# Optimization experiments

Measured on AMD Instinct MI355X. Metric: run time of the kernel, lower is better.

## Reference

```python
import jax, jax.numpy as jnp
import numpy as np

N_NODES = 50000
N_EDGES = 1600000
IN_FEAT = 256
HIDDEN = 128
N_CLASSES = 16


def gcn_conv(x, edge_index, W, b, n_nodes):
    """PyG GCNConv: x' = D^{-1/2} (A+I) D^{-1/2} (x @ W) + b."""
    h = x @ W  # project first (PyG order), messages are in out_dim
    src, dst = edge_index[0], edge_index[1]
    loops = jnp.arange(n_nodes, dtype=src.dtype)
    src = jnp.concatenate([src, loops])
    dst = jnp.concatenate([dst, loops])
    # degree of A+I (count incoming edges incl. self loop)
    deg = jax.ops.segment_sum(jnp.ones_like(dst, dtype=h.dtype), dst, num_segments=n_nodes)
    dis = jax.lax.rsqrt(deg)  # deg >= 1 thanks to self loops
    norm = dis[src] * dis[dst]  # [E+N]
    msgs = h[src] * norm[:, None]  # gather + scale
    out = jax.ops.segment_sum(msgs, dst, num_segments=n_nodes)  # scatter-add
    return out + b


def setup_inputs() -> dict:
    key = jax.random.key(0)
    k_x, k_e, k_w1, k_b1, k_w2, k_b2 = jax.random.split(key, 6)
    x = jax.random.normal(k_x, (N_NODES, IN_FEAT), dtype=jnp.float32)
    edge_index = jax.random.randint(k_e, (2, N_EDGES), 0, N_NODES, dtype=jnp.int64)
    s1 = 1.0 / np.sqrt(IN_FEAT)
    s2 = 1.0 / np.sqrt(HIDDEN)
    W1 = jax.random.uniform(k_w1, (IN_FEAT, HIDDEN), jnp.float32, -s1, s1)
    b1 = jax.random.uniform(k_b1, (HIDDEN,), jnp.float32, -s1, s1)
    W2 = jax.random.uniform(k_w2, (HIDDEN, N_CLASSES), jnp.float32, -s2, s2)
    b2 = jax.random.uniform(k_b2, (N_CLASSES,), jnp.float32, -s2, s2)
    return {"x": x, "edge_index": edge_index, "W1": W1, "b1": b1, "W2": W2, "b2": b2}


def reference(x, edge_index, W1, b1, W2, b2):
    n = x.shape[0]
    h = gcn_conv(x, edge_index, W1, b1, n)
    h = jax.nn.relu(h)
    logits = gcn_conv(h, edge_index, W2, b2, n)
    return logits, jax.nn.softmax(logits, axis=1)
```

## Files before the change

### kernel.cpp

```cpp
#include <hip/hip_runtime.h>
#include <hip/hip_bf16.h>
#include <math.h>

#define N_NODES 50000
#define N_EDGES 1600000
#define IN_FEAT 256
#define HIDDEN 128
#define N_CLASSES 16

#define ECHUNK 8192
#define NCHK 196
#define NBKT 196
#define BCAP 10240

typedef __attribute__((ext_vector_type(8))) short short8;
typedef __attribute__((ext_vector_type(4))) float floatx4;

__device__ __forceinline__ unsigned short f2bf(float f) {
    unsigned u = __float_as_uint(f);
    return (unsigned short)((u + 0x7fffu + ((u >> 16) & 1u)) >> 16);
}

__device__ __forceinline__ unsigned pk2bf(float a, float b) {
    __hip_bfloat162 h = __float22bfloat162_rn(make_float2(a, b));
    union { __hip_bfloat162 h; unsigned u; } cv;
    cv.h = h;
    return cv.u;
}

__device__ __forceinline__ float bflo(unsigned u) { return __uint_as_float(u << 16); }
__device__ __forceinline__ float bfhi(unsigned u) { return __uint_as_float(u & 0xffff0000u); }

__global__ __launch_bounds__(256) void scatter_edges2(const int* __restrict__ src,
                                                      const int* __restrict__ dst,
                                                      int* __restrict__ cursor,
                                                      unsigned int* __restrict__ sorted,
                                                      const float* __restrict__ W1,
                                                      unsigned short* __restrict__ w1t) {
    __shared__ int hloc[256];
    int t = threadIdx.x;
    hloc[t] = 0;
    if (blockIdx.x < HIDDEN)
        w1t[blockIdx.x * IN_FEAT + t] = f2bf(W1[t * HIDDEN + blockIdx.x]);
    __syncthreads();
    int base = blockIdx.x * ECHUNK;
    int end = min(base + ECHUNK, N_EDGES);
    for (int i = base + t; i < end; i += 256)
        atomicAdd(&hloc[dst[i] >> 8], 1);
    __syncthreads();
    int cnt = hloc[t];
    int lbase = t * BCAP + atomicAdd(&cursor[t], cnt);
    __syncthreads();
    hloc[t] = lbase;
    __syncthreads();
    for (int i = base + t; i < end; i += 256) {
        int d = dst[i];
        int s = src[i];
        int pos = atomicAdd(&hloc[d >> 8], 1);
        sorted[pos] = ((unsigned)d << 16) | (unsigned)s;
    }
}

__global__ __launch_bounds__(256) void build_csr2(const unsigned int* __restrict__ sorted,
                                                  const int* __restrict__ cursor,
                                                  int* __restrict__ rs,
                                                  int* __restrict__ re,
                                                  float* __restrict__ dis,
                                                  unsigned short* __restrict__ csr_src) {
    __shared__ int cnt[256];
    __shared__ int roff[256];
    int t = threadIdx.x;
    int bkt = blockIdx.x;
    int ebase = bkt * BCAP;
    int eend = ebase + cursor[bkt];
    cnt[t] = 0;
    __syncthreads();
    for (int i = ebase + t; i < eend; i += 256)
        atomicAdd(&cnt[(sorted[i] >> 16) & 255], 1);
    __syncthreads();
    int v = cnt[t];
    roff[t] = v;
    __syncthreads();
    for (int off = 1; off < 256; off <<= 1) {
        int x = (t >= off) ? roff[t - off] : 0;
        __syncthreads();
        roff[t] += x;
        __syncthreads();
    }
    int excl = roff[t] - v;
    int node = bkt * 256 + t;
    if (node < N_NODES) {
        rs[node] = ebase + excl;
        re[node] = ebase + excl + v;
        dis[node] = 1.0f / sqrtf((float)(v + 1));
    }
    __syncthreads();
    cnt[t] = ebase + excl;
    __syncthreads();
    for (int i = ebase + t; i < eend; i += 256) {
        unsigned e = sorted[i];
        int pos = atomicAdd(&cnt[(e >> 16) & 255], 1);
        csr_src[pos] = (unsigned short)(e & 0xffffu);
    }
}

#define XCH 260

__global__ __launch_bounds__(256) void gemm1_mfma(const float* __restrict__ x,
                                                  const unsigned short* __restrict__ w1t,
                                                  const float* __restrict__ dis,
                                                  unsigned int* __restrict__ g1) {
    __shared__ float xs[2][8 * XCH];
    int tid = threadIdx.x;
    int w = tid >> 6;
    int lane = tid & 63;
    int quad = lane >> 4;
    int c = lane & 15;
    int row_base = blockIdx.x * 64;
    int wrow = (w >> 1) * 32;
    int col_base = (w & 1) * 64;

    int st_row = min(row_base + 16 * w + (lane >> 3), N_NODES - 1);
    int st_row2 = min(row_base + 16 * w + 8 + (lane >> 3), N_NODES - 1);
    const float* gp1 = x + (size_t)st_row * IN_FEAT + (lane & 7) * 4;
    const float* gp2 = x + (size_t)st_row2 * IN_FEAT + (lane & 7) * 4;

    floatx4 acc[2][4] = {};
    const unsigned short* bp[4];
#pragma unroll
    for (int nt = 0; nt < 4; ++nt)
        bp[nt] = w1t + (size_t)(col_base + nt * 16 + c) * IN_FEAT + quad * 8;

    int dwoff[2];
#pragma unroll
    for (int rt = 0; rt < 2; ++rt) {
        int rit = wrow + rt * 16 + c;
        dwoff[rt] = (rit >> 3) * XCH + (rit & 7) * 32 + quad * 8;
    }

#define STAGE(buf, k0)                                                                  \
    do {                                                                                \
        __builtin_amdgcn_global_load_lds(                                               \
            (const __attribute__((address_space(1))) void*)(gp1 + (k0)),                \
            (__attribute__((address_space(3))) void*)&xs[buf][(2 * w) * XCH], 16, 0, 0);\
        __builtin_amdgcn_global_load_lds(                                               \
            (const __attribute__((address_space(1))) void*)(gp2 + (k0)),                \
            (__attribute__((address_space(3))) void*)&xs[buf][(2 * w + 1) * XCH], 16, 0, 0);\
    } while (0)

    STAGE(0, 0);
    __syncthreads();

    int buf = 0;
#pragma unroll
    for (int kk = 0; kk < 8; ++kk) {
        if (kk < 7) STAGE(buf ^ 1, (kk + 1) * 32);
        short8 b[4];
#pragma unroll
        for (int nt = 0; nt < 4; ++nt)
            b[nt] = *(const short8*)(bp[nt] + kk * 32);
        short8 a[2];
#pragma unroll
        for (int rt = 0; rt < 2; ++rt) {
            float4 f0 = *(const float4*)&xs[buf][dwoff[rt]];
            float4 f1 = *(const float4*)&xs[buf][dwoff[rt] + 4];
            union { short8 s; unsigned u[4]; } au;
            au.u[0] = pk2bf(f0.x, f0.y);
            au.u[1] = pk2bf(f0.z, f0.w);
            au.u[2] = pk2bf(f1.x, f1.y);
            au.u[3] = pk2bf(f1.z, f1.w);
            a[rt] = au.s;
        }
#pragma unroll
        for (int rt = 0; rt < 2; ++rt)
#pragma unroll
            for (int nt = 0; nt < 4; ++nt)
                acc[rt][nt] = __builtin_amdgcn_mfma_f32_16x16x32_bf16(a[rt], b[nt], acc[rt][nt], 0, 0, 0);
        __syncthreads();
        buf ^= 1;
    }
#undef STAGE

    bool evenlane = (lane & 1) == 0;
#pragma unroll
    for (int rt = 0; rt < 2; ++rt) {
#pragma unroll
        for (int reg = 0; reg < 4; ++reg) {
            int row = row_base + wrow + rt * 16 + quad * 4 + reg;
            float dv = dis[min(row, N_NODES - 1)];
#pragma unroll
            for (int nt = 0; nt < 4; ++nt) {
                float v = acc[rt][nt][reg] * dv;
                float vo = __shfl_xor(v, 1);
                if (evenlane && row < N_NODES) {
                    unsigned pkd = (unsigned)f2bf(v) | ((unsigned)f2bf(vo) << 16);
                    g1[(size_t)row * 64 + (col_base >> 1) + nt * 8 + (c >> 1)] = pkd;
                }
            }
        }
    }
}

__global__ __launch_bounds__(256) void agg1_gemm2(const unsigned int* __restrict__ g1,
                                                  const int* __restrict__ rs,
                                                  const int* __restrict__ re,
                                                  const unsigned short* __restrict__ csr_src,
                                                  const float* __restrict__ dis,
                                                  const float* __restrict__ b1,
                                                  const float* __restrict__ W2,
                                                  float* __restrict__ g2) {
    __shared__ float w2s[HIDDEN * N_CLASSES];
    __shared__ float rsh[4][HIDDEN];
    int tid = threadIdx.x;
    for (int i = tid; i < HIDDEN * N_CLASSES; i += 256) w2s[i] = W2[i];
    __syncthreads();

    int wave = tid >> 6;
    int lane = tid & 63;
    int hi = lane >> 5;
    int m = lane & 31;
    int node = blockIdx.x * 4 + wave;
    const uint2* g = (const uint2*)g1;

    float s0 = 0.f, s1 = 0.f, s2 = 0.f, s3 = 0.f;
    float t0 = 0.f, t1 = 0.f, t2 = 0.f, t3 = 0.f;
    if (hi == 0) {
        uint2 su = g[(size_t)node * 32 + m];
        s0 = bflo(su.x); s1 = bfhi(su.x); s2 = bflo(su.y); s3 = bfhi(su.y);
    }

    int e0 = rs[node], e1 = re[node];
    int e = e0;
    for (; e + 16 <= e1; e += 16) {
        int i0 = csr_src[e + 0 + hi], i1 = csr_src[e + 2 + hi];
        int i2 = csr_src[e + 4 + hi], i3 = csr_src[e + 6 + hi];
        int i4 = csr_src[e + 8 + hi], i5 = csr_src[e + 10 + hi];
        int i6 = csr_src[e + 12 + hi], i7 = csr_src[e + 14 + hi];
        uint2 u0 = g[(size_t)i0 * 32 + m];
        uint2 u1 = g[(size_t)i1 * 32 + m];
        uint2 u2 = g[(size_t)i2 * 32 + m];
        uint2 u3 = g[(size_t)i3 * 32 + m];
        uint2 u4 = g[(size_t)i4 * 32 + m];
        uint2 u5 = g[(size_t)i5 * 32 + m];
        uint2 u6 = g[(size_t)i6 * 32 + m];
        uint2 u7 = g[(size_t)i7 * 32 + m];
        s0 += bflo(u0.x); s1 += bfhi(u0.x); s2 += bflo(u0.y); s3 += bfhi(u0.y);
        t0 += bflo(u1.x); t1 += bfhi(u1.x); t2 += bflo(u1.y); t3 += bfhi(u1.y);
        s0 += bflo(u2.x); s1 += bfhi(u2.x); s2 += bflo(u2.y); s3 += bfhi(u2.y);
        t0 += bflo(u3.x); t1 += bfhi(u3.x); t2 += bflo(u3.y); t3 += bfhi(u3.y);
        s0 += bflo(u4.x); s1 += bfhi(u4.x); s2 += bflo(u4.y); s3 += bfhi(u4.y);
        t0 += bflo(u5.x); t1 += bfhi(u5.x); t2 += bflo(u5.y); t3 += bfhi(u5.y);
        s0 += bflo(u6.x); s1 += bfhi(u6.x); s2 += bflo(u6.y); s3 += bfhi(u6.y);
        t0 += bflo(u7.x); t1 += bfhi(u7.x); t2 += bflo(u7.y); t3 += bfhi(u7.y);
    }
    for (; e + 2 <= e1; e += 2) {
        int i0 = csr_src[e + hi];
        uint2 u = g[(size_t)i0 * 32 + m];
        s0 += bflo(u.x); s1 += bfhi(u.x); s2 += bflo(u.y); s3 += bfhi(u.y);
    }
    if (e < e1 && hi == 0) {
        int i0 = csr_src[e];
        uint2 u = g[(size_t)i0 * 32 + m];
        s0 += bflo(u.x); s1 += bfhi(u.x); s2 += bflo(u.y); s3 += bfhi(u.y);
    }
    s0 += t0; s1 += t1; s2 += t2; s3 += t3;
    s0 += __shfl_xor(s0, 32);
    s1 += __shfl_xor(s1, 32);
    s2 += __shfl_xor(s2, 32);
    s3 += __shfl_xor(s3, 32);

    float dv = dis[node];
    if (hi == 0) {
        float4 bb = *(const float4*)&b1[4 * m];
        float4 r;
        r.x = fmaxf(fmaf(dv, s0, bb.x), 0.f);
        r.y = fmaxf(fmaf(dv, s1, bb.y), 0.f);
        r.z = fmaxf(fmaf(dv, s2, bb.z), 0.f);
        r.w = fmaxf(fmaf(dv, s3, bb.w), 0.f);
        *(float4*)&rsh[wave][4 * m] = r;
    }

    int grp = lane >> 4;
    int c = lane & 15;
    int f0 = grp * 32;
    float p = 0.f;
#pragma unroll
    for (int k = 0; k < 32; ++k)
        p = fmaf(rsh[wave][f0 + k], w2s[(f0 + k) * N_CLASSES + c], p);
    p += __shfl_xor(p, 16);
    p += __shfl_xor(p, 32);
    if (lane < 16) g2[(size_t)node * N_CLASSES + lane] = dv * p;
}

__global__ __launch_bounds__(256) void agg2_softmax(const float* __restrict__ g2,
                                                    const int* __restrict__ rs,
                                                    const int* __restrict__ re,
                                                    const unsigned short* __restrict__ csr_src,
                                                    const float* __restrict__ dis,
                                                    const float* __restrict__ b2,
                                                    float* __restrict__ out) {
    int tid = threadIdx.x;
    int node = blockIdx.x * 16 + (tid >> 4);
    int c = tid & 15;
    float acc0 = g2[(size_t)node * N_CLASSES + c];
    float acc1 = 0.f, acc2 = 0.f, acc3 = 0.f;
    float acc4 = 0.f, acc5 = 0.f, acc6 = 0.f, acc7 = 0.f;
    int e0 = rs[node], e1 = re[node];
    int e = e0;
    for (; e + 8 <= e1; e += 8) {
        int s0 = csr_src[e + 0], s1 = csr_src[e + 1], s2 = csr_src[e + 2], s3 = csr_src[e + 3];
        int s4 = csr_src[e + 4], s5 = csr_src[e + 5], s6 = csr_src[e + 6], s7 = csr_src[e + 7];
        acc0 += g2[(size_t)s0 * N_CLASSES + c];
        acc1 += g2[(size_t)s1 * N_CLASSES + c];
        acc2 += g2[(size_t)s2 * N_CLASSES + c];
        acc3 += g2[(size_t)s3 * N_CLASSES + c];
        acc4 += g2[(size_t)s4 * N_CLASSES + c];
        acc5 += g2[(size_t)s5 * N_CLASSES + c];
        acc6 += g2[(size_t)s6 * N_CLASSES + c];
        acc7 += g2[(size_t)s7 * N_CLASSES + c];
    }
    for (; e < e1; ++e) {
        int s = csr_src[e];
        acc0 += g2[(size_t)s * N_CLASSES + c];
    }
    acc0 = ((acc0 + acc1) + (acc2 + acc3)) + ((acc4 + acc5) + (acc6 + acc7));
    float logit = fmaf(dis[node], acc0, b2[c]);
    out[(size_t)node * N_CLASSES + c] = logit;
    float m = logit;
    for (int off = 8; off; off >>= 1) m = fmaxf(m, __shfl_xor(m, off));
    float ex = expf(logit - m);
    float s = ex;
    for (int off = 8; off; off >>= 1) s += __shfl_xor(s, off);
    out[(size_t)N_NODES * N_CLASSES + (size_t)node * N_CLASSES + c] = ex / s;
}


extern "C" void kernel_launch(void* const* d_in, const int* in_sizes, int n_in,
                              void* d_out, int out_size, void* d_ws, size_t ws_size,
                              hipStream_t stream) {
    const float* x  = (const float*)d_in[0];
    const int*   ei = (const int*)d_in[1];
    const float* W1 = (const float*)d_in[2];
    const float* b1 = (const float*)d_in[3];
    const float* W2 = (const float*)d_in[4];
    const float* b2 = (const float*)d_in[5];
    float* out = (float*)d_out;

    char* ws = (char*)d_ws;
    size_t off = 0;
    auto alloc = [&](size_t bytes) -> char* {
        char* p = ws + off;
        off = (off + bytes + 511) & ~(size_t)511;
        return p;
    };
    int*   cursor   = (int*)alloc(256 * 4);
    float* dis      = (float*)alloc(N_NODES * 4);
    int*   rs       = (int*)alloc(N_NODES * 4);
    int*   re       = (int*)alloc(N_NODES * 4);
    unsigned short* w1t = (unsigned short*)alloc((size_t)HIDDEN * IN_FEAT * 2);
    unsigned short* csr_src = (unsigned short*)alloc((size_t)NBKT * BCAP * 2);
    unsigned int* g1 = (unsigned int*)alloc((size_t)N_NODES * 64 * 4);
    float* g2       = (float*)alloc((size_t)N_NODES * N_CLASSES * 4);
    unsigned int* sorted = (unsigned int*)g1;
    (void)ws_size; (void)in_sizes; (void)n_in; (void)out_size;

    const int* src = ei;
    const int* dst = ei + N_EDGES;

    hipMemsetAsync(cursor, 0, 256 * 4, stream);
    scatter_edges2<<<NCHK, 256, 0, stream>>>(src, dst, cursor, sorted, W1, w1t);
    build_csr2<<<NBKT, 256, 0, stream>>>(sorted, cursor, rs, re, dis, csr_src);

    gemm1_mfma<<<(N_NODES + 63) / 64, 256, 0, stream>>>(x, w1t, dis, g1);
    agg1_gemm2<<<N_NODES / 4, 256, 0, stream>>>(g1, rs, re, csr_src, dis, b1, W2, g2);
    agg2_softmax<<<N_NODES / 16, 256, 0, stream>>>(g2, rs, re, csr_src, dis, b2, out);
}
```

Baseline: 240.7 us.

## Overlap CSR fill with gemm1 and widen per-node parallelism in layer-2 aggregation

Splits CSR construction into a count pass and a fill pass, then runs the fill pass as extra blocks of the gemm1 launch so the CSR scatter overlaps the projection GEMM. This needs a separate buffer for the sorted edges, which previously reused g1's memory. agg2_softmax now gives each node a full wave, with four 16-lane groups striding over its edges and a shuffle reduction, which raises memory-level parallelism in the gather. The costs are extra workspace and a wave per node where only 16 lanes do the softmax.

```diff
diff --git a/kernel.cpp b/kernel.cpp
--- a/kernel.cpp
+++ b/kernel.cpp
@@ -12,6 +12,7 @@
 #define NCHK 196
 #define NBKT 196
 #define BCAP 10240
+#define GEMM1_BLKS 782
 
 typedef __attribute__((ext_vector_type(8))) short short8;
 typedef __attribute__((ext_vector_type(4))) float floatx4;
@@ -61,12 +62,11 @@
     }
 }
 
-__global__ __launch_bounds__(256) void build_csr2(const unsigned int* __restrict__ sorted,
-                                                  const int* __restrict__ cursor,
-                                                  int* __restrict__ rs,
-                                                  int* __restrict__ re,
-                                                  float* __restrict__ dis,
-                                                  unsigned short* __restrict__ csr_src) {
+__global__ __launch_bounds__(256) void build_counts(const unsigned int* __restrict__ sorted,
+                                                    const int* __restrict__ cursor,
+                                                    int* __restrict__ rs,
+                                                    int* __restrict__ re,
+                                                    float* __restrict__ dis) {
     __shared__ int cnt[256];
     __shared__ int roff[256];
     int t = threadIdx.x;
@@ -94,29 +94,44 @@
         re[node] = ebase + excl + v;
         dis[node] = 1.0f / sqrtf((float)(v + 1));
     }
-    __syncthreads();
-    cnt[t] = ebase + excl;
-    __syncthreads();
-    for (int i = ebase + t; i < eend; i += 256) {
-        unsigned e = sorted[i];
-        int pos = atomicAdd(&cnt[(e >> 16) & 255], 1);
-        csr_src[pos] = (unsigned short)(e & 0xffffu);
-    }
 }
 
 #define XCH 260
 
-__global__ __launch_bounds__(256) void gemm1_mfma(const float* __restrict__ x,
-                                                  const unsigned short* __restrict__ w1t,
-                                                  const float* __restrict__ dis,
-                                                  unsigned int* __restrict__ g1) {
+__global__ __launch_bounds__(256) void fill_and_gemm1(const unsigned int* __restrict__ sorted,
+                                                      const int* __restrict__ cursor,
+                                                      const int* __restrict__ rs,
+                                                      unsigned short* __restrict__ csr_src,
+                                                      const float* __restrict__ x,
+                                                      const unsigned short* __restrict__ w1t,
+                                                      const float* __restrict__ dis,
+                                                      unsigned int* __restrict__ g1) {
     __shared__ float xs[2][8 * XCH];
     int tid = threadIdx.x;
+
+    if (blockIdx.x < NBKT) {
+        int* cnt = (int*)&xs[0][0];
+        int t = tid;
+        int bkt = blockIdx.x;
+        int ebase = bkt * BCAP;
+        int eend = ebase + cursor[bkt];
+        int node = bkt * 256 + t;
+        cnt[t] = (node < N_NODES) ? rs[node] : 0;
+        __syncthreads();
+        for (int i = ebase + t; i < eend; i += 256) {
+            unsigned e = sorted[i];
+            int pos = atomicAdd(&cnt[(e >> 16) & 255], 1);
+            csr_src[pos] = (unsigned short)(e & 0xffffu);
+        }
+        return;
+    }
+
+    int bid = blockIdx.x - NBKT;
     int w = tid >> 6;
     int lane = tid & 63;
     int quad = lane >> 4;
     int c = lane & 15;
-    int row_base = blockIdx.x * 64;
+    int row_base = bid * 64;
     int wrow = (w >> 1) * 32;
     int col_base = (w & 1) * 64;
 
@@ -300,38 +315,51 @@
                                                     const float* __restrict__ b2,
                                                     float* __restrict__ out) {
     int tid = threadIdx.x;
-    int node = blockIdx.x * 16 + (tid >> 4);
-    int c = tid & 15;
-    float acc0 = g2[(size_t)node * N_CLASSES + c];
+    int wave = tid >> 6;
+    int lane = tid & 63;
+    int grp = lane >> 4;
+    int c = lane & 15;
+    int node = blockIdx.x * 4 + wave;
+
+    float acc0 = (grp == 0) ? g2[(size_t)node * N_CLASSES + c] : 0.f;
     float acc1 = 0.f, acc2 = 0.f, acc3 = 0.f;
     float acc4 = 0.f, acc5 = 0.f, acc6 = 0.f, acc7 = 0.f;
     int e0 = rs[node], e1 = re[node];
     int e = e0;
-    for (; e + 8 <= e1; e += 8) {
-        int s0 = csr_src[e + 0], s1 = csr_src[e + 1], s2 = csr_src[e + 2], s3 = csr_src[e + 3];
-        int s4 = csr_src[e + 4], s5 = csr_src[e + 5], s6 = csr_src[e + 6], s7 = csr_src[e + 7];
-        acc0 += g2[(size_t)s0 * N_CLASSES + c];
-        acc1 += g2[(size_t)s1 * N_CLASSES + c];
-        acc2 += g2[(size_t)s2 * N_CLASSES + c];
-        acc3 += g2[(size_t)s3 * N_CLASSES + c];
-        acc4 += g2[(size_t)s4 * N_CLASSES + c];
-        acc5 += g2[(size_t)s5 * N_CLASSES + c];
-        acc6 += g2[(size_t)s6 * N_CLASSES + c];
-        acc7 += g2[(size_t)s7 * N_CLASSES + c];
-    }
-    for (; e < e1; ++e) {
-        int s = csr_src[e];
-        acc0 += g2[(size_t)s * N_CLASSES + c];
-    }
-    acc0 = ((acc0 + acc1) + (acc2 + acc3)) + ((acc4 + acc5) + (acc6 + acc7));
-    float logit = fmaf(dis[node], acc0, b2[c]);
-    out[(size_t)node * N_CLASSES + c] = logit;
+    for (; e + 32 <= e1; e += 32) {
+        int i0 = csr_src[e + grp], i1 = csr_src[e + 4 + grp];
+        int i2 = csr_src[e + 8 + grp], i3 = csr_src[e + 12 + grp];
+        int i4 = csr_src[e + 16 + grp], i5 = csr_src[e + 20 + grp];
+        int i6 = csr_src[e + 24 + grp], i7 = csr_src[e + 28 + grp];
+        acc0 += g2[(size_t)i0 * N_CLASSES + c];
+        acc1 += g2[(size_t)i1 * N_CLASSES + c];
+        acc2 += g2[(size_t)i2 * N_CLASSES + c];
+        acc3 += g2[(size_t)i3 * N_CLASSES + c];
+        acc4 += g2[(size_t)i4 * N_CLASSES + c];
+        acc5 += g2[(size_t)i5 * N_CLASSES + c];
+        acc6 += g2[(size_t)i6 * N_CLASSES + c];
+        acc7 += g2[(size_t)i7 * N_CLASSES + c];
+    }
+    for (; e + 4 <= e1; e += 4) {
+        int i = csr_src[e + grp];
+        acc1 += g2[(size_t)i * N_CLASSES + c];
+    }
+    if (e + grp < e1) {
+        int i = csr_src[e + grp];
+        acc2 += g2[(size_t)i * N_CLASSES + c];
+    }
+    float sum = ((acc0 + acc1) + (acc2 + acc3)) + ((acc4 + acc5) + (acc6 + acc7));
+    sum += __shfl_xor(sum, 16);
+    sum += __shfl_xor(sum, 32);
+
+    float logit = fmaf(dis[node], sum, b2[c]);
+    if (lane < 16) out[(size_t)node * N_CLASSES + c] = logit;
     float m = logit;
     for (int off = 8; off; off >>= 1) m = fmaxf(m, __shfl_xor(m, off));
     float ex = expf(logit - m);
     float s = ex;
     for (int off = 8; off; off >>= 1) s += __shfl_xor(s, off);
-    out[(size_t)N_NODES * N_CLASSES + (size_t)node * N_CLASSES + c] = ex / s;
+    if (lane < 16) out[(size_t)N_NODES * N_CLASSES + (size_t)node * N_CLASSES + c] = ex / s;
 }
 
 
@@ -359,9 +387,9 @@
     int*   re       = (int*)alloc(N_NODES * 4);
     unsigned short* w1t = (unsigned short*)alloc((size_t)HIDDEN * IN_FEAT * 2);
     unsigned short* csr_src = (unsigned short*)alloc((size_t)NBKT * BCAP * 2);
+    unsigned int* sorted = (unsigned int*)alloc((size_t)NBKT * BCAP * 4);
     unsigned int* g1 = (unsigned int*)alloc((size_t)N_NODES * 64 * 4);
     float* g2       = (float*)alloc((size_t)N_NODES * N_CLASSES * 4);
-    unsigned int* sorted = (unsigned int*)g1;
     (void)ws_size; (void)in_sizes; (void)n_in; (void)out_size;
 
     const int* src = ei;
@@ -369,9 +397,9 @@
 
     hipMemsetAsync(cursor, 0, 256 * 4, stream);
     scatter_edges2<<<NCHK, 256, 0, stream>>>(src, dst, cursor, sorted, W1, w1t);
-    build_csr2<<<NBKT, 256, 0, stream>>>(sorted, cursor, rs, re, dis, csr_src);
-
-    gemm1_mfma<<<(N_NODES + 63) / 64, 256, 0, stream>>>(x, w1t, dis, g1);
+    build_counts<<<NBKT, 256, 0, stream>>>(sorted, cursor, rs, re, dis);
+    fill_and_gemm1<<<NBKT + GEMM1_BLKS, 256, 0, stream>>>(sorted, cursor, rs, csr_src,
+                                                          x, w1t, dis, g1);
     agg1_gemm2<<<N_NODES / 4, 256, 0, stream>>>(g1, rs, re, csr_src, dis, b1, W2, g2);
-    agg2_softmax<<<N_NODES / 16, 256, 0, stream>>>(g2, rs, re, csr_src, dis, b2, out);
-}
+    agg2_softmax<<<N_NODES / 4, 256, 0, stream>>>(g2, rs, re, csr_src, dis, b2, out);
+}
```

New measurement: 246.4 us. +2.4%, slower.
